# Kernel tuning notes

Measured on AMD Instinct MI355X. Metric: run time of the kernel, lower is better.

Reference implementation:

```python
import jax, jax.numpy as jnp
import numpy as np

DIM = 96       # d_model / channels
DSTATE = 16    # SSM state size N
DINNER = 2 * DIM   # expand=2 -> 192
DTRANK = 6     # ceil(DIM/16)
K = 4          # scan directions
B, H, W = 2, 56, 56


def _ln(x, g, b, eps=1e-5):
    m = x.mean(-1, keepdims=True)
    v = x.var(-1, keepdims=True)
    return (x - m) * jax.lax.rsqrt(v + eps) * g + b


def _dwconv3(x, w, b):  # x [B,C,H,W], w [C,1,3,3] depthwise, SAME padding
    y = jax.lax.conv_general_dilated(x, w, (1, 1), [(1, 1), (1, 1)],
                                     feature_group_count=x.shape[1],
                                     dimension_numbers=('NCHW', 'OIHW', 'NCHW'))
    return y + b[None, :, None, None]


def _bn(x, g, b, m, v, eps=1e-5):  # eval-mode BatchNorm2d on NCHW
    inv = jax.lax.rsqrt(v + eps)
    return (x - m[None, :, None, None]) * (inv * g)[None, :, None, None] + b[None, :, None, None]


def _selective_scan(u, dt, A, Bs, Cs, Dp, dt_bias):
    # u, dt: [B,K,D,L]; A: [K,D,N]; Bs,Cs: [B,K,N,L]; Dp, dt_bias: [K,D]
    dt = jax.nn.softplus(dt + dt_bias[None, :, :, None])
    dA = jnp.exp(jnp.einsum('bkdl,kdn->lbkdn', dt, A))           # [L,B,K,D,N]
    dBu = jnp.einsum('bkdl,bknl,bkdl->lbkdn', dt, Bs, u)          # [L,B,K,D,N]
    Ct = jnp.moveaxis(Cs, -1, 0)                                  # [L,B,K,N]
    h0 = jnp.zeros(dA.shape[1:], dA.dtype)

    def step(h, inp):
        dA_l, dBu_l, C_l = inp
        h = dA_l * h + dBu_l
        return h, jnp.einsum('bkdn,bkn->bkd', h, C_l)

    _, ys = jax.lax.scan(step, h0, (dA, dBu, Ct))                 # ys [L,B,K,D]
    return jnp.moveaxis(ys, 0, -1) + u * Dp[None, :, :, None]     # [B,K,D,L]


def setup_inputs() -> dict:
    key = jax.random.key(0)
    ks = jax.random.split(key, 12)
    s = 0.02
    f32 = jnp.float32
    inp = {}
    inp['x'] = jax.random.normal(ks[0], (B, H, W, DIM), f32)
    # conv branch: depthwise 3x3 + BN + ReLU + 1x1 + BN
    inp['dw_w'] = jax.random.normal(ks[1], (DIM, 1, 3, 3), f32) * s
    inp['dw_b'] = jnp.zeros((DIM,), f32)
    inp['bn1_g'] = jnp.ones((DIM,), f32); inp['bn1_b'] = jnp.zeros((DIM,), f32)
    inp['bn1_m'] = jnp.zeros((DIM,), f32); inp['bn1_v'] = jnp.ones((DIM,), f32)
    inp['pw_w'] = jax.random.normal(ks[2], (DIM, DIM), f32) * s
    inp['pw_b'] = jnp.zeros((DIM,), f32)
    inp['bn2_g'] = jnp.ones((DIM,), f32); inp['bn2_b'] = jnp.zeros((DIM,), f32)
    inp['bn2_m'] = jnp.zeros((DIM,), f32); inp['bn2_v'] = jnp.ones((DIM,), f32)
    # pre-mamba LayerNorm
    inp['ln_g'] = jnp.ones((DIM,), f32); inp['ln_b'] = jnp.zeros((DIM,), f32)
    # SS2D params
    inp['in_proj_w'] = jax.random.normal(ks[3], (2 * DINNER, DIM), f32) * s
    inp['conv_w'] = jax.random.normal(ks[4], (DINNER, 1, 3, 3), f32) * s
    inp['conv_b'] = jnp.zeros((DINNER,), f32)
    inp['x_proj_w'] = jax.random.normal(ks[5], (K, DTRANK + 2 * DSTATE, DINNER), f32) * s
    inp['dt_w'] = jax.random.normal(ks[6], (K, DINNER, DTRANK), f32) * s
    inp['dt_b'] = jnp.full((K, DINNER), -4.6, f32)  # softplus(dt_b) ~= 0.01
    inp['A_logs'] = jnp.log(jnp.tile(jnp.arange(1, DSTATE + 1, dtype=f32), (K * DINNER, 1)))
    inp['Ds'] = jnp.ones((K * DINNER,), f32)
    inp['out_norm_g'] = jnp.ones((DINNER,), f32); inp['out_norm_b'] = jnp.zeros((DINNER,), f32)
    inp['out_proj_w'] = jax.random.normal(ks[7], (DIM, DINNER), f32) * s
    # fusion: Linear(2*dim, dim) + LayerNorm(dim)
    inp['fus_w'] = jax.random.normal(ks[8], (DIM, 2 * DIM), f32) * s
    inp['fus_b'] = jnp.zeros((DIM,), f32)
    inp['fus_ln_g'] = jnp.ones((DIM,), f32); inp['fus_ln_b'] = jnp.zeros((DIM,), f32)
    return inp


def reference(x, dw_w, dw_b, bn1_g, bn1_b, bn1_m, bn1_v, pw_w, pw_b,
              bn2_g, bn2_b, bn2_m, bn2_v, ln_g, ln_b,
              in_proj_w, conv_w, conv_b, x_proj_w, dt_w, dt_b, A_logs, Ds,
              out_norm_g, out_norm_b, out_proj_w, fus_w, fus_b, fus_ln_g, fus_ln_b):
    Bsz, Hh, Ww, C = x.shape
    L = Hh * Ww
    # ----- conv branch -----
    xc = jnp.transpose(x, (0, 3, 1, 2))                       # [B,C,H,W]
    c = jax.nn.relu(_bn(_dwconv3(xc, dw_w, dw_b), bn1_g, bn1_b, bn1_m, bn1_v))
    c = jnp.einsum('bchw,oc->bohw', c, pw_w) + pw_b[None, :, None, None]
    conv_out = jnp.transpose(_bn(c, bn2_g, bn2_b, bn2_m, bn2_v), (0, 2, 3, 1))
    # ----- mamba (SS2D) branch -----
    xn = _ln(x, ln_g, ln_b)
    xz = xn @ in_proj_w.T                                     # [B,H,W,2*Din]
    xm, z = jnp.split(xz, 2, axis=-1)
    xm = jnp.transpose(xm, (0, 3, 1, 2))                      # [B,Din,H,W]
    xm = jax.nn.silu(_dwconv3(xm, conv_w, conv_b))
    v1 = xm.reshape(Bsz, DINNER, L)                           # row-major scan
    v2 = jnp.transpose(xm, (0, 1, 3, 2)).reshape(Bsz, DINNER, L)  # col-major scan
    xs = jnp.stack([v1, v2, v1[..., ::-1], v2[..., ::-1]], axis=1)  # [B,4,Din,L]
    x_dbl = jnp.einsum('bkdl,kcd->bkcl', xs, x_proj_w)
    dts, Bmat, Cmat = jnp.split(x_dbl, [DTRANK, DTRANK + DSTATE], axis=2)
    dts = jnp.einsum('bkrl,kdr->bkdl', dts, dt_w)
    A = -jnp.exp(A_logs).reshape(K, DINNER, DSTATE)
    out_y = _selective_scan(xs, dts, A, Bmat, Cmat, Ds.reshape(K, DINNER), dt_b)
    y1 = out_y[:, 0]
    inv_y = out_y[:, 2:4][..., ::-1]
    y2 = inv_y[:, 0]
    y3 = jnp.transpose(inv_y[:, 1].reshape(Bsz, DINNER, Ww, Hh), (0, 1, 3, 2)).reshape(Bsz, DINNER, L)
    y4 = jnp.transpose(out_y[:, 1].reshape(Bsz, DINNER, Ww, Hh), (0, 1, 3, 2)).reshape(Bsz, DINNER, L)
    y = jnp.transpose(y1 + y2 + y3 + y4, (0, 2, 1)).reshape(Bsz, Hh, Ww, DINNER)
    y = _ln(y, out_norm_g, out_norm_b)
    y = y * jax.nn.silu(z)
    mamba_out = y @ out_proj_w.T                              # [B,H,W,C]
    # ----- fusion + residual -----
    fused = jnp.concatenate([conv_out, mamba_out], axis=-1) @ fus_w.T + fus_b
    fused = _ln(fused, fus_ln_g, fus_ln_b)
    return x + fused
```

## Files before the change

kernel.cpp:

```cpp
#include <hip/hip_runtime.h>
#include <math.h>

#define BZ 2
#define HH 56
#define WW 56
#define LL 3136
#define CC 96
#define DI 192
#define NS 16
#define RR 6
#define NT 49
#define NC 49

#define OFF_CONV   0
#define OFF_XMRAW  602112
#define OFF_Z      1806336
#define OFF_V1     3010560
#define OFF_V2     4214784
#define OFF_DT     5419008
#define OFF_BS     10235904
#define OFF_CS     10637312
#define OFF_Y      11038720
#define OFF_Y13    15855616
#define OFF_T      18264064
#define OFF_W2     19468288

__device__ __forceinline__ float softplusf(float x) {
    if (x > 20.f) return x;
    return log1pf(__expf(x));
}

__global__ __launch_bounds__(64) void k0_w2(const float* __restrict__ fus_w,
                                            const float* __restrict__ opw,
                                            float* __restrict__ W2) {
    int i = blockIdx.x * 64 + threadIdx.x;
    if (i >= CC * DI) return;
    int o = i / DI, d = i % DI;
    float acc = 0.f;
    for (int j = 0; j < CC; ++j)
        acc += fus_w[o * DI + CC + j] * opw[j * DI + d];
    W2[i] = acc;
}

__global__ __launch_bounds__(256) void k0c_negA(const float* __restrict__ A_logs,
                                                float* __restrict__ negA) {
    int i = blockIdx.x * 256 + threadIdx.x;
    if (i < 4 * DI * NS) negA[i] = -__expf(A_logs[i]);
}

__global__ __launch_bounds__(256) void k1a_dw(const float* __restrict__ x,
    const float* __restrict__ dw_w, const float* __restrict__ dw_b,
    const float* __restrict__ bn1_g, const float* __restrict__ bn1_b,
    const float* __restrict__ bn1_m, const float* __restrict__ bn1_v,
    float* __restrict__ cbuf) {
    int i = blockIdx.x * 256 + threadIdx.x;
    if (i >= BZ * LL * CC) return;
    int c = i % CC;
    int bl = i / CC;
    int l = bl % LL, b = bl / LL;
    int h = l / WW, w = l % WW;
    float acc = dw_b[c];
    #pragma unroll
    for (int dy = -1; dy <= 1; ++dy) {
        int hh = h + dy; if (hh < 0 || hh >= HH) continue;
        #pragma unroll
        for (int dx = -1; dx <= 1; ++dx) {
            int ww = w + dx; if (ww < 0 || ww >= WW) continue;
            acc += x[((b * HH + hh) * WW + ww) * CC + c] * dw_w[c * 9 + (dy + 1) * 3 + (dx + 1)];
        }
    }
    float inv = rsqrtf(bn1_v[c] + 1e-5f);
    float v = (acc - bn1_m[c]) * inv * bn1_g[c] + bn1_b[c];
    cbuf[i] = fmaxf(v, 0.f);
}

__global__ __launch_bounds__(256) void k1b_pw(const float* __restrict__ cbuf,
    const float* __restrict__ pw_w, const float* __restrict__ pw_b,
    const float* __restrict__ bn2_g, const float* __restrict__ bn2_b,
    const float* __restrict__ bn2_m, const float* __restrict__ bn2_v,
    float* __restrict__ conv_out) {
    int t0 = blockIdx.x * 64;
    int b = blockIdx.y;
    int lane = threadIdx.x & 63;
    int wvu = __builtin_amdgcn_readfirstlane(threadIdx.x >> 6);
    __shared__ float ct[CC * 65];
    __shared__ float res[64 * 97];
    const float* cb = cbuf + (b * LL + t0) * CC;
    for (int e = threadIdx.x; e < 64 * CC; e += 256) {
        int p = e / CC, c = e % CC;
        ct[c * 65 + p] = cb[e];
    }
    __syncthreads();
    float acc[24];
    const float* pb = pw_b + wvu * 24;
    #pragma unroll
    for (int j = 0; j < 24; ++j) acc[j] = pb[j];
    const float* wb = pw_w + (wvu * 24) * CC;
    for (int c = 0; c < CC; ++c) {
        float xv = ct[c * 65 + lane];
        #pragma unroll
        for (int j = 0; j < 24; ++j)
            acc[j] += xv * wb[j * CC + c];
    }
    #pragma unroll
    for (int j = 0; j < 24; ++j) {
        int o = wvu * 24 + j;
        float inv = rsqrtf(bn2_v[o] + 1e-5f);
        res[lane * 97 + o] = (acc[j] - bn2_m[o]) * inv * bn2_g[o] + bn2_b[o];
    }
    __syncthreads();
    float* ob = conv_out + (b * LL + t0) * CC;
    for (int e = threadIdx.x; e < 64 * CC; e += 256) {
        int pl = e / CC, o = e % CC;
        ob[e] = res[pl * 97 + o];
    }
}

__global__ __launch_bounds__(256) void k2_inproj(const float* __restrict__ x,
    const float* __restrict__ ln_g, const float* __restrict__ ln_b,
    const float* __restrict__ ipw,
    float* __restrict__ xm_raw, float* __restrict__ z_buf) {
    int t0 = blockIdx.x * 64;
    int og = blockIdx.y;
    int b = blockIdx.z;
    int lane = threadIdx.x & 63;
    int wv = threadIdx.x >> 6;
    int wvu = __builtin_amdgcn_readfirstlane(wv);
    __shared__ float xt[64 * 97];
    __shared__ float xn[96 * 65];
    __shared__ float ps[4][64], ps2[4][64];
    const float* xb = x + (b * LL + t0) * CC;
    for (int e = threadIdx.x; e < 64 * CC; e += 256) {
        int p = e / CC, c = e % CC;
        xt[p * 97 + c] = xb[e];
    }
    __syncthreads();
    float s = 0.f, s2 = 0.f;
    #pragma unroll
    for (int j = 0; j < 24; ++j) {
        float v = xt[lane * 97 + wvu * 24 + j];
        s += v; s2 += v * v;
    }
    ps[wv][lane] = s; ps2[wv][lane] = s2;
    __syncthreads();
    float st = 0.f, st2 = 0.f;
    #pragma unroll
    for (int i = 0; i < 4; ++i) { st += ps[i][lane]; st2 += ps2[i][lane]; }
    float m = st * (1.f / 96.f);
    float inv = rsqrtf(st2 * (1.f / 96.f) - m * m + 1e-5f);
    #pragma unroll
    for (int j = 0; j < 24; ++j) {
        int c = wvu * 24 + j;
        xn[c * 65 + lane] = (xt[lane * 97 + c] - m) * inv * ln_g[c] + ln_b[c];
    }
    __syncthreads();
    float acc[24];
    #pragma unroll
    for (int j = 0; j < 24; ++j) acc[j] = 0.f;
    const float* wbase = ipw + (og * 96 + wvu * 24) * CC;
    for (int c = 0; c < CC; ++c) {
        float xv = xn[c * 65 + lane];
        #pragma unroll
        for (int j = 0; j < 24; ++j)
            acc[j] += xv * wbase[j * CC + c];
    }
    int p = t0 + lane;
    #pragma unroll
    for (int j = 0; j < 24; ++j) {
        int out = og * 96 + wvu * 24 + j;
        if (out < DI) xm_raw[(b * DI + out) * LL + p] = acc[j];
        else          z_buf[(b * DI + (out - DI)) * LL + p] = acc[j];
    }
}

__global__ __launch_bounds__(256) void k3_dw(const float* __restrict__ xm_raw,
    const float* __restrict__ conv_w, const float* __restrict__ conv_b,
    float* __restrict__ v1, float* __restrict__ v2) {
    int bd = blockIdx.x;
    int half = blockIdx.y;
    int d = bd % DI;
    int h0 = half * 28;
    __shared__ float tile[28 * 57];
    const float* src = xm_raw + bd * LL;
    float wloc[9];
    #pragma unroll
    for (int i = 0; i < 9; ++i) wloc[i] = conv_w[d * 9 + i];
    float bias = conv_b[d];
    for (int e = threadIdx.x; e < 28 * WW; e += 256) {
        int hl = e / WW, w = e % WW;
        int h = h0 + hl;
        float acc = bias;
        #pragma unroll
        for (int dy = -1; dy <= 1; ++dy) {
            int hh = h + dy; if (hh < 0 || hh >= HH) continue;
            #pragma unroll
            for (int dx = -1; dx <= 1; ++dx) {
                int ww = w + dx; if (ww < 0 || ww >= WW) continue;
                acc += src[hh * WW + ww] * wloc[(dy + 1) * 3 + (dx + 1)];
            }
        }
        float sig = 1.f / (1.f + __expf(-acc));
        float v = acc * sig;
        v1[bd * LL + h * WW + w] = v;
        tile[hl * 57 + w] = v;
    }
    __syncthreads();
    for (int e = threadIdx.x; e < 28 * WW; e += 256) {
        int w = e / 28, hl = e % 28;
        v2[bd * LL + w * HH + h0 + hl] = tile[hl * 57 + w];
    }
}

__global__ __launch_bounds__(256) void k4_proj(const float* __restrict__ v1,
    const float* __restrict__ v2, const float* __restrict__ xpw,
    const float* __restrict__ dtw, const float* __restrict__ dtb,
    float* __restrict__ dt_s, float* __restrict__ B_s, float* __restrict__ C_s) {
    int t0 = blockIdx.x * 64;
    int k = blockIdx.y;
    int b = blockIdx.z;
    int lane = threadIdx.x & 63;
    int wvu = __builtin_amdgcn_readfirstlane(threadIdx.x >> 6);
    __shared__ float xs_l[DI * 64];
    __shared__ float dtr[RR * 64];
    const float* src = ((k & 1) == 0 ? v1 : v2) + b * DI * LL + t0;
    for (int e = threadIdx.x; e < DI * 64; e += 256) {
        int d = e >> 6, p = e & 63;
        xs_l[e] = src[d * LL + p];
    }
    __syncthreads();
    int r0 = wvu * 10; if (r0 > 28) r0 = 28;
    float acc[10];
    #pragma unroll
    for (int i = 0; i < 10; ++i) acc[i] = 0.f;
    const float* wbase = xpw + (k * 38 + r0) * DI;
    for (int d = 0; d < DI; ++d) {
        float xv = xs_l[d * 64 + lane];
        #pragma unroll
        for (int i = 0; i < 10; ++i)
            acc[i] += xv * wbase[i * DI + d];
    }
    int p = t0 + lane;
    #pragma unroll
    for (int i = 0; i < 10; ++i) {
        int c = r0 + i;
        if (c < RR) {
            dtr[c * 64 + lane] = acc[i];
        } else if (c < RR + NS) {
            B_s[((b * 4 + k) * NS + (c - RR)) * LL + p] = acc[i];
        } else {
            C_s[((b * 4 + k) * NS + (c - RR - NS)) * LL + p] = acc[i];
        }
    }
    __syncthreads();
    for (int i = 0; i < 48; ++i) {
        int d = wvu * 48 + i;
        float a = dtb[k * DI + d];
        const float* wr = dtw + (k * DI + d) * RR;
        #pragma unroll
        for (int r = 0; r < RR; ++r)
            a += dtr[r * 64 + lane] * wr[r];
        dt_s[((b * 4 + k) * DI + d) * LL + p] = softplusf(a);
    }
}

__global__ __launch_bounds__(64) void k5a_scan(float* __restrict__ dt_s,
    const float* __restrict__ B_s, const float* __restrict__ C_s,
    const float* __restrict__ v1, const float* __restrict__ v2,
    const float* __restrict__ A_logs, float* __restrict__ y_scan,
    float* __restrict__ hlast) {
    int bx = blockIdx.x;
    int dg = bx % 3, c = bx / 3;
    int k = blockIdx.y, b = blockIdx.z;
    int bk = b * 4 + k;
    int lane = threadIdx.x;
    int d0 = dg * 64, d = d0 + lane;
    bool fwd = (k < 2);
    int s0 = fwd ? c * 64 : (LL - (c + 1) * 64);
    __shared__ float dt_l[64 * 65];
    __shared__ float u_l[64 * 65];
    __shared__ float4 bc4[64 * 9];
    float* bc = (float*)bc4;
    float Ae[16];
    const float* ap = A_logs + (k * DI + d) * NS;
    #pragma unroll
    for (int n = 0; n < 16; ++n) Ae[n] = -__expf(ap[n]) * 1.442695040888963f;
    const float* dtp = dt_s + (bk * DI + d0) * LL + s0;
    const float* up  = ((k == 0 || k == 2) ? v1 : v2) + (b * DI + d0) * LL + s0;
    #pragma unroll 8
    for (int r = 0; r < 64; ++r) {
        dt_l[r * 65 + lane] = dtp[r * LL + lane];
        u_l[r * 65 + lane]  = up[r * LL + lane];
    }
    const float* Bb = B_s + (bk * NS) * LL + s0;
    const float* Cb = C_s + (bk * NS) * LL + s0;
    #pragma unroll
    for (int n = 0; n < 16; ++n) {
        bc[lane * 36 + n]      = Bb[n * LL + lane];
        bc[lane * 36 + 16 + n] = Cb[n * LL + lane];
    }
    __syncthreads();
    float h[16];
    #pragma unroll
    for (int n = 0; n < 16; ++n) h[n] = 0.f;
    float cum = 0.f;
    for (int jj = 0; jj < 64; ++jj) {
        int j = fwd ? jj : 63 - jj;
        float dtv = dt_l[lane * 65 + j];
        float uv  = u_l[lane * 65 + j];
        float du = dtv * uv;
        cum += dtv;
        const float4* row = (const float4*)&bc[j * 36];
        float4 b0 = row[0], b1 = row[1], b2 = row[2], b3 = row[3];
        float4 c0 = row[4], c1 = row[5], c2 = row[6], c3 = row[7];
        float bv[16] = {b0.x,b0.y,b0.z,b0.w, b1.x,b1.y,b1.z,b1.w,
                        b2.x,b2.y,b2.z,b2.w, b3.x,b3.y,b3.z,b3.w};
        float cv[16] = {c0.x,c0.y,c0.z,c0.w, c1.x,c1.y,c1.z,c1.w,
                        c2.x,c2.y,c2.z,c2.w, c3.x,c3.y,c3.z,c3.w};
        float y = 0.f;
        #pragma unroll
        for (int n = 0; n < 16; ++n) {
            h[n] = exp2f(dtv * Ae[n]) * h[n] + du * bv[n];
            y += h[n] * cv[n];
        }
        u_l[lane * 65 + j] = y;
        dt_l[lane * 65 + j] = cum;
    }
    __syncthreads();
    float* yp = y_scan + (bk * DI + d0) * LL + s0;
    float* cp = dt_s + (bk * DI + d0) * LL + s0;
    #pragma unroll 8
    for (int r = 0; r < 64; ++r) {
        yp[r * LL + lane] = u_l[r * 65 + lane];
        cp[r * LL + lane] = dt_l[r * 65 + lane];
    }
    float4* hp4 = (float4*)(hlast + (bk * NC + c) * (DI * NS) + d * NS);
    hp4[0] = make_float4(h[0], h[1], h[2], h[3]);
    hp4[1] = make_float4(h[4], h[5], h[6], h[7]);
    hp4[2] = make_float4(h[8], h[9], h[10], h[11]);
    hp4[3] = make_float4(h[12], h[13], h[14], h[15]);
}

__global__ __launch_bounds__(64) void k5c_comb(const float* __restrict__ hlast,
    const float* __restrict__ cumdt, const float* __restrict__ negA,
    float* __restrict__ hin) {
    int dg = blockIdx.x, k = blockIdx.y, b = blockIdx.z;
    int lane = threadIdx.x, dl = lane >> 4, n = lane & 15;
    int d = dg * 4 + dl;
    int bk = b * 4 + k;
    bool fwd = (k < 2);
    float Av = negA[(k * DI + d) * NS + n];
    float H = 0.f;
    for (int c = 0; c < NC; ++c) {
        hin[(bk * NC + c) * (48 * 64) + dg * 64 + lane] = H;
        int s0 = fwd ? c * 64 : (LL - (c + 1) * 64);
        int jlast = fwd ? s0 + 63 : s0;
        float T = cumdt[(bk * DI + d) * LL + jlast];
        float hl = hlast[(bk * NC + c) * (48 * 64) + dg * 64 + lane];
        H = hl + __expf(Av * T) * H;
    }
}

__global__ __launch_bounds__(256) void k5d_corr(const float* __restrict__ cumdt,
    const float* __restrict__ C_s, const float* __restrict__ hin,
    const float* __restrict__ negA, float* __restrict__ y_scan) {
    int t = blockIdx.x;
    int k = blockIdx.y, b = blockIdx.z;
    bool fwd = (k < 2);
    int tile = fwd ? (t + 1) : t;
    int c = fwd ? tile : (48 - tile);
    int s0 = tile * 64;
    int lane = threadIdx.x & 63;
    int wvu = __builtin_amdgcn_readfirstlane(threadIdx.x >> 6);
    int bk = b * 4 + k;
    __shared__ float c_l[16 * 65];
    for (int e = threadIdx.x; e < 16 * 64; e += 256) {
        int n = e >> 6, s = e & 63;
        c_l[n * 65 + s] = C_s[(bk * NS + n) * LL + s0 + s];
    }
    __syncthreads();
    for (int dd = 0; dd < 48; ++dd) {
        int d = wvu * 48 + dd;
        float cd = cumdt[(bk * DI + d) * LL + s0 + lane];
        const float* hp = hin + (bk * NC + c) * (48 * 64) + d * 16;
        const float* ap = negA + (k * DI + d) * NS;
        float acc = 0.f;
        #pragma unroll
        for (int n = 0; n < 16; ++n) {
            acc += c_l[n * 65 + lane] * __expf(ap[n] * cd) * hp[n];
        }
        y_scan[(bk * DI + d) * LL + s0 + lane] += acc;
    }
}

__global__ __launch_bounds__(64) void k5b_tr(const float* __restrict__ y_scan,
                                             float* __restrict__ y13t) {
    int idx = blockIdx.x;
    int d = idx % DI;
    int bk = idx / DI;
    int kk = bk % 2, b = bk / 2;
    int k = (kk == 0) ? 1 : 3;
    __shared__ float tile[HH * 57];
    const float* src = y_scan + ((b * 4 + k) * DI + d) * LL;
    for (int e = threadIdx.x; e < LL; e += 64) {
        int w = e / HH, h = e % HH;
        tile[h * 57 + w] = src[e];
    }
    __syncthreads();
    float* dst = y13t + idx * LL;
    for (int e = threadIdx.x; e < LL; e += 64) {
        int h = e / WW, w = e % WW;
        dst[e] = tile[h * 57 + w];
    }
}

__global__ __launch_bounds__(256) void k6_gather(const float* __restrict__ y_scan,
    const float* __restrict__ y13t, const float* __restrict__ v1,
    const float* __restrict__ z_buf, const float* __restrict__ Ds,
    const float* __restrict__ ong, const float* __restrict__ onb,
    float* __restrict__ t_buf) {
    int t0 = blockIdx.x * 32;
    int b = blockIdx.y;
    int p32 = threadIdx.x & 31, sl = threadIdx.x >> 5;
    int p = t0 + p32;
    __shared__ float yv[DI * 33];
    __shared__ float ps[8][32], ps2[8][32];
    float s = 0.f, s2 = 0.f;
    for (int j = 0; j < 24; ++j) {
        int d = sl * 24 + j;
        float dsum = Ds[d] + Ds[DI + d] + Ds[2 * DI + d] + Ds[3 * DI + d];
        float val = y_scan[((b * 4 + 0) * DI + d) * LL + p]
                  + y_scan[((b * 4 + 2) * DI + d) * LL + p]
                  + y13t[((b * 2 + 0) * DI + d) * LL + p]
                  + y13t[((b * 2 + 1) * DI + d) * LL + p]
                  + v1[(b * DI + d) * LL + p] * dsum;
        yv[d * 33 + p32] = val;
        s += val; s2 += val * val;
    }
    ps[sl][p32] = s; ps2[sl][p32] = s2;
    __syncthreads();
    float st = 0.f, st2 = 0.f;
    #pragma unroll
    for (int i = 0; i < 8; ++i) { st += ps[i][p32]; st2 += ps2[i][p32]; }
    float m = st * (1.f / 192.f);
    float inv = rsqrtf(st2 * (1.f / 192.f) - m * m + 1e-5f);
    for (int j = 0; j < 24; ++j) {
        int d = sl * 24 + j;
        float val = (yv[d * 33 + p32] - m) * inv * ong[d] + onb[d];
        float zz = z_buf[(b * DI + d) * LL + p];
        float sig = 1.f / (1.f + __expf(-zz));
        t_buf[(b * DI + d) * LL + p] = val * zz * sig;
    }
}

__global__ __launch_bounds__(256) void k7a_mm(const float* __restrict__ t_buf,
    const float* __restrict__ conv_out, const float* __restrict__ W2,
    const float* __restrict__ fus_w, const float* __restrict__ fus_b,
    float* __restrict__ fusedT) {
    int t0 = blockIdx.x * 64;
    int og = blockIdx.y;
    int b = blockIdx.z;
    int lane = threadIdx.x & 63;
    int wvu = __builtin_amdgcn_readfirstlane(threadIdx.x >> 6);
    __shared__ float ct[CC * 65];
    const float* cb = conv_out + (b * LL + t0) * CC;
    for (int e = threadIdx.x; e < 64 * CC; e += 256) {
        int p = e / CC, c = e % CC;
        ct[c * 65 + p] = cb[e];
    }
    __syncthreads();
    int o0 = og * 24 + wvu * 6;
    float acc[6];
    #pragma unroll
    for (int j = 0; j < 6; ++j) acc[j] = fus_b[o0 + j];
    int p = t0 + lane;
    const float* w2 = W2 + o0 * DI;
    for (int d = 0; d < DI; ++d) {
        float tv = t_buf[(b * DI + d) * LL + p];
        #pragma unroll
        for (int j = 0; j < 6; ++j)
            acc[j] += tv * w2[j * DI + d];
    }
    const float* fw = fus_w + o0 * DI;
    for (int c = 0; c < CC; ++c) {
        float cv = ct[c * 65 + lane];
        #pragma unroll
        for (int j = 0; j < 6; ++j)
            acc[j] += cv * fw[j * DI + c];
    }
    #pragma unroll
    for (int j = 0; j < 6; ++j)
        fusedT[(b * CC + o0 + j) * LL + p] = acc[j];
}

__global__ __launch_bounds__(256) void k7b_ln(const float* __restrict__ fusedT,
    const float* __restrict__ flg, const float* __restrict__ flb,
    const float* __restrict__ x, float* __restrict__ out) {
    int t0 = blockIdx.x * 64;
    int b = blockIdx.y;
    int lane = threadIdx.x & 63, wv = threadIdx.x >> 6;
    __shared__ float ft[CC * 65];
    __shared__ float res[64 * 97];
    __shared__ float ps[4][64], ps2[4][64];
    for (int e = threadIdx.x; e < CC * 64; e += 256) {
        int o = e >> 6, p = e & 63;
        ft[o * 65 + p] = fusedT[(b * CC + o) * LL + t0 + p];
    }
    __syncthreads();
    float s = 0.f, s2 = 0.f;
    #pragma unroll
    for (int j = 0; j < 24; ++j) {
        float v = ft[(wv * 24 + j) * 65 + lane];
        s += v; s2 += v * v;
    }
    ps[wv][lane] = s; ps2[wv][lane] = s2;
    __syncthreads();
    float st = 0.f, st2 = 0.f;
    #pragma unroll
    for (int i = 0; i < 4; ++i) { st += ps[i][lane]; st2 += ps2[i][lane]; }
    float m = st * (1.f / 96.f);
    float inv = rsqrtf(st2 * (1.f / 96.f) - m * m + 1e-5f);
    #pragma unroll
    for (int j = 0; j < 24; ++j) {
        int o = wv * 24 + j;
        res[lane * 97 + o] = (ft[o * 65 + lane] - m) * inv * flg[o] + flb[o];
    }
    __syncthreads();
    const float* xb = x + (b * LL + t0) * CC;
    float* ob = out + (b * LL + t0) * CC;
    for (int e = threadIdx.x; e < 64 * CC; e += 256) {
        int pl = e / CC, o = e % CC;
        ob[e] = xb[e] + res[pl * 97 + o];
    }
}

extern "C" void kernel_launch(void* const* d_in, const int* in_sizes, int n_in,
                              void* d_out, int out_size, void* d_ws, size_t ws_size,
                              hipStream_t stream) {
    const float* x        = (const float*)d_in[0];
    const float* dw_w     = (const float*)d_in[1];
    const float* dw_b     = (const float*)d_in[2];
    const float* bn1_g    = (const float*)d_in[3];
    const float* bn1_b    = (const float*)d_in[4];
    const float* bn1_m    = (const float*)d_in[5];
    const float* bn1_v    = (const float*)d_in[6];
    const float* pw_w     = (const float*)d_in[7];
    const float* pw_b     = (const float*)d_in[8];
    const float* bn2_g    = (const float*)d_in[9];
    const float* bn2_b    = (const float*)d_in[10];
    const float* bn2_m    = (const float*)d_in[11];
    const float* bn2_v    = (const float*)d_in[12];
    const float* ln_g     = (const float*)d_in[13];
    const float* ln_b     = (const float*)d_in[14];
    const float* ipw      = (const float*)d_in[15];
    const float* conv_w   = (const float*)d_in[16];
    const float* conv_b   = (const float*)d_in[17];
    const float* xpw      = (const float*)d_in[18];
    const float* dtw      = (const float*)d_in[19];
    const float* dtb      = (const float*)d_in[20];
    const float* A_logs   = (const float*)d_in[21];
    const float* Ds       = (const float*)d_in[22];
    const float* ong      = (const float*)d_in[23];
    const float* onb      = (const float*)d_in[24];
    const float* opw      = (const float*)d_in[25];
    const float* fus_w    = (const float*)d_in[26];
    const float* fus_b    = (const float*)d_in[27];
    const float* flg      = (const float*)d_in[28];
    const float* flb      = (const float*)d_in[29];

    float* ws = (float*)d_ws;
    float* conv_out = ws + OFF_CONV;
    float* xm_raw   = ws + OFF_XMRAW;
    float* z_buf    = ws + OFF_Z;
    float* v1       = ws + OFF_V1;
    float* v2       = ws + OFF_V2;
    float* dt_s     = ws + OFF_DT;
    float* B_s      = ws + OFF_BS;
    float* C_s      = ws + OFF_CS;
    float* y_scan   = ws + OFF_Y;
    float* y13t     = ws + OFF_Y13;
    float* t_buf    = ws + OFF_T;
    float* W2       = ws + OFF_W2;
    float* hlast    = xm_raw;
    float* hin      = t_buf;
    float* negA     = B_s;
    float* cbuf     = y13t;
    float* fusedT   = y13t;
    float* out      = (float*)d_out;

    k0_w2<<<dim3((CC * DI + 63) / 64), dim3(64), 0, stream>>>(fus_w, opw, W2);
    k1a_dw<<<dim3((BZ * LL * CC + 255) / 256), dim3(256), 0, stream>>>(x, dw_w, dw_b,
                                                     bn1_g, bn1_b, bn1_m, bn1_v, cbuf);
    k1b_pw<<<dim3(NT, BZ), dim3(256), 0, stream>>>(cbuf, pw_w, pw_b,
                                                   bn2_g, bn2_b, bn2_m, bn2_v, conv_out);
    k2_inproj<<<dim3(NT, 4, BZ), dim3(256), 0, stream>>>(x, ln_g, ln_b, ipw, xm_raw, z_buf);
    k3_dw<<<dim3(BZ * DI, 2), dim3(256), 0, stream>>>(xm_raw, conv_w, conv_b, v1, v2);
    k4_proj<<<dim3(NT, 4, BZ), dim3(256), 0, stream>>>(v1, v2, xpw, dtw, dtb, dt_s, B_s, C_s);
    k5a_scan<<<dim3(3 * NC, 4, BZ), dim3(64), 0, stream>>>(dt_s, B_s, C_s, v1, v2, A_logs, y_scan, hlast);
    k0c_negA<<<dim3(48), dim3(256), 0, stream>>>(A_logs, negA);
    k5c_comb<<<dim3(48, 4, BZ), dim3(64), 0, stream>>>(hlast, dt_s, negA, hin);
    k5d_corr<<<dim3(48, 4, BZ), dim3(256), 0, stream>>>(dt_s, C_s, hin, negA, y_scan);
    k5b_tr<<<dim3(BZ * 2 * DI), dim3(64), 0, stream>>>(y_scan, y13t);
    k6_gather<<<dim3(2 * NT, BZ), dim3(256), 0, stream>>>(y_scan, y13t, v1, z_buf, Ds, ong, onb, t_buf);
    k7a_mm<<<dim3(NT, 4, BZ), dim3(256), 0, stream>>>(t_buf, conv_out, W2, fus_w, fus_b, fusedT);
    k7b_ln<<<dim3(NT, BZ), dim3(256), 0, stream>>>(fusedT, flg, flb, x, out);
}
```

Measured before the change: 381.0 us.

## Halve scan chunk length and recompute cumulative dt in correction pass

The chunked selective scan now uses 32-step chunks instead of 64, doubling the number of scan blocks and shortening each block's serial dependency chain. Chunk carry-out states are written into a larger reused buffer along with a single per-chunk dt total, so the scan no longer writes a full cumulative-dt array. The correction kernel rebuilds the in-chunk cumulative dt with a wave-level shuffle prefix sum. The combine kernel's serial pass doubles in length, and the transpose kernel moves to 256 threads.

```diff
diff --git a/kernel.cpp b/kernel.cpp
--- a/kernel.cpp
+++ b/kernel.cpp
@@ -10,7 +10,8 @@
 #define NS 16
 #define RR 6
 #define NT 49
-#define NC 49
+#define NCH 98
+#define CH 32
 
 #define OFF_CONV   0
 #define OFF_XMRAW  602112
@@ -263,11 +264,11 @@
     }
 }
 
-__global__ __launch_bounds__(64) void k5a_scan(float* __restrict__ dt_s,
+__global__ __launch_bounds__(64) void k5a_scan(const float* __restrict__ dt_s,
     const float* __restrict__ B_s, const float* __restrict__ C_s,
     const float* __restrict__ v1, const float* __restrict__ v2,
     const float* __restrict__ A_logs, float* __restrict__ y_scan,
-    float* __restrict__ hlast) {
+    float* __restrict__ hl_buf, float* __restrict__ Tbuf) {
     int bx = blockIdx.x;
     int dg = bx % 3, c = bx / 3;
     int k = blockIdx.y, b = blockIdx.z;
@@ -275,43 +276,43 @@
     int lane = threadIdx.x;
     int d0 = dg * 64, d = d0 + lane;
     bool fwd = (k < 2);
-    int s0 = fwd ? c * 64 : (LL - (c + 1) * 64);
-    __shared__ float dt_l[64 * 65];
-    __shared__ float u_l[64 * 65];
-    __shared__ float4 bc4[64 * 9];
-    float* bc = (float*)bc4;
+    int s0 = fwd ? c * CH : (LL - (c + 1) * CH);
+    __shared__ float dtl[64 * 33];
+    __shared__ float ul[64 * 33];
+    __shared__ float bc[CH * 36];
     float Ae[16];
     const float* ap = A_logs + (k * DI + d) * NS;
     #pragma unroll
     for (int n = 0; n < 16; ++n) Ae[n] = -__expf(ap[n]) * 1.442695040888963f;
     const float* dtp = dt_s + (bk * DI + d0) * LL + s0;
-    const float* up  = ((k == 0 || k == 2) ? v1 : v2) + (b * DI + d0) * LL + s0;
+    const float* up  = ((k & 1) == 0 ? v1 : v2) + (b * DI + d0) * LL + s0;
+    int pr = lane >> 5, pc = lane & 31;
     #pragma unroll 8
-    for (int r = 0; r < 64; ++r) {
-        dt_l[r * 65 + lane] = dtp[r * LL + lane];
-        u_l[r * 65 + lane]  = up[r * LL + lane];
-    }
-    const float* Bb = B_s + (bk * NS) * LL + s0;
-    const float* Cb = C_s + (bk * NS) * LL + s0;
-    #pragma unroll
-    for (int n = 0; n < 16; ++n) {
-        bc[lane * 36 + n]      = Bb[n * LL + lane];
-        bc[lane * 36 + 16 + n] = Cb[n * LL + lane];
+    for (int i = 0; i < 32; ++i) {
+        int row = i * 2 + pr;
+        dtl[row * 33 + pc] = dtp[row * LL + pc];
+        ul[row * 33 + pc]  = up[row * LL + pc];
+    }
+    #pragma unroll
+    for (int i = 0; i < 8; ++i) {
+        int nn = i * 2 + pr;
+        bc[pc * 36 + nn]      = B_s[(bk * NS + nn) * LL + s0 + pc];
+        bc[pc * 36 + 16 + nn] = C_s[(bk * NS + nn) * LL + s0 + pc];
     }
     __syncthreads();
     float h[16];
     #pragma unroll
     for (int n = 0; n < 16; ++n) h[n] = 0.f;
     float cum = 0.f;
-    for (int jj = 0; jj < 64; ++jj) {
-        int j = fwd ? jj : 63 - jj;
-        float dtv = dt_l[lane * 65 + j];
-        float uv  = u_l[lane * 65 + j];
+    for (int jj = 0; jj < CH; ++jj) {
+        int j = fwd ? jj : CH - 1 - jj;
+        float dtv = dtl[lane * 33 + j];
+        float uv  = ul[lane * 33 + j];
         float du = dtv * uv;
         cum += dtv;
-        const float4* row = (const float4*)&bc[j * 36];
-        float4 b0 = row[0], b1 = row[1], b2 = row[2], b3 = row[3];
-        float4 c0 = row[4], c1 = row[5], c2 = row[6], c3 = row[7];
+        const float4* row4 = (const float4*)&bc[j * 36];
+        float4 b0 = row4[0], b1 = row4[1], b2 = row4[2], b3 = row4[3];
+        float4 c0 = row4[4], c1 = row4[5], c2 = row4[6], c3 = row4[7];
         float bv[16] = {b0.x,b0.y,b0.z,b0.w, b1.x,b1.y,b1.z,b1.w,
                         b2.x,b2.y,b2.z,b2.w, b3.x,b3.y,b3.z,b3.w};
         float cv[16] = {c0.x,c0.y,c0.z,c0.w, c1.x,c1.y,c1.z,c1.w,
@@ -322,78 +323,86 @@
             h[n] = exp2f(dtv * Ae[n]) * h[n] + du * bv[n];
             y += h[n] * cv[n];
         }
-        u_l[lane * 65 + j] = y;
-        dt_l[lane * 65 + j] = cum;
+        ul[lane * 33 + j] = y;
     }
     __syncthreads();
     float* yp = y_scan + (bk * DI + d0) * LL + s0;
-    float* cp = dt_s + (bk * DI + d0) * LL + s0;
     #pragma unroll 8
-    for (int r = 0; r < 64; ++r) {
-        yp[r * LL + lane] = u_l[r * 65 + lane];
-        cp[r * LL + lane] = dt_l[r * 65 + lane];
-    }
-    float4* hp4 = (float4*)(hlast + (bk * NC + c) * (DI * NS) + d * NS);
+    for (int i = 0; i < 32; ++i) {
+        int row = i * 2 + pr;
+        yp[row * LL + pc] = ul[row * 33 + pc];
+    }
+    float4* hp4 = (float4*)(hl_buf + (bk * NCH + c) * (DI * NS) + d * NS);
     hp4[0] = make_float4(h[0], h[1], h[2], h[3]);
     hp4[1] = make_float4(h[4], h[5], h[6], h[7]);
     hp4[2] = make_float4(h[8], h[9], h[10], h[11]);
     hp4[3] = make_float4(h[12], h[13], h[14], h[15]);
-}
-
-__global__ __launch_bounds__(64) void k5c_comb(const float* __restrict__ hlast,
-    const float* __restrict__ cumdt, const float* __restrict__ negA,
-    float* __restrict__ hin) {
+    Tbuf[(bk * NCH + c) * DI + d] = cum;
+}
+
+__global__ __launch_bounds__(64) void k5c_comb(float* __restrict__ hl_buf,
+    const float* __restrict__ Tbuf, const float* __restrict__ negA) {
     int dg = blockIdx.x, k = blockIdx.y, b = blockIdx.z;
     int lane = threadIdx.x, dl = lane >> 4, n = lane & 15;
     int d = dg * 4 + dl;
     int bk = b * 4 + k;
-    bool fwd = (k < 2);
     float Av = negA[(k * DI + d) * NS + n];
     float H = 0.f;
-    for (int c = 0; c < NC; ++c) {
-        hin[(bk * NC + c) * (48 * 64) + dg * 64 + lane] = H;
-        int s0 = fwd ? c * 64 : (LL - (c + 1) * 64);
-        int jlast = fwd ? s0 + 63 : s0;
-        float T = cumdt[(bk * DI + d) * LL + jlast];
-        float hl = hlast[(bk * NC + c) * (48 * 64) + dg * 64 + lane];
+    for (int c = 0; c < NCH; ++c) {
+        float* slot = hl_buf + (bk * NCH + c) * (DI * NS) + dg * 64 + lane;
+        float hl = *slot;
+        *slot = H;
+        float T = Tbuf[(bk * NCH + c) * DI + d];
         H = hl + __expf(Av * T) * H;
     }
 }
 
-__global__ __launch_bounds__(256) void k5d_corr(const float* __restrict__ cumdt,
+__global__ __launch_bounds__(256) void k5d_corr(const float* __restrict__ dt_s,
     const float* __restrict__ C_s, const float* __restrict__ hin,
     const float* __restrict__ negA, float* __restrict__ y_scan) {
     int t = blockIdx.x;
     int k = blockIdx.y, b = blockIdx.z;
     bool fwd = (k < 2);
-    int tile = fwd ? (t + 1) : t;
-    int c = fwd ? tile : (48 - tile);
-    int s0 = tile * 64;
-    int lane = threadIdx.x & 63;
-    int wvu = __builtin_amdgcn_readfirstlane(threadIdx.x >> 6);
+    int c  = fwd ? (t + 1) : (NCH - 1 - t);
+    int s0 = fwd ? (t + 1) * CH : t * CH;
+    int p32 = threadIdx.x & 31, sl = threadIdx.x >> 5;
     int bk = b * 4 + k;
-    __shared__ float c_l[16 * 65];
-    for (int e = threadIdx.x; e < 16 * 64; e += 256) {
-        int n = e >> 6, s = e & 63;
-        c_l[n * 65 + s] = C_s[(bk * NS + n) * LL + s0 + s];
-    }
-    __syncthreads();
-    for (int dd = 0; dd < 48; ++dd) {
-        int d = wvu * 48 + dd;
-        float cd = cumdt[(bk * DI + d) * LL + s0 + lane];
-        const float* hp = hin + (bk * NC + c) * (48 * 64) + d * 16;
+    __shared__ float c_l[16 * 33];
+    for (int e = threadIdx.x; e < 16 * CH; e += 256) {
+        int n = e >> 5, s = e & 31;
+        c_l[n * 33 + s] = C_s[(bk * NS + n) * LL + s0 + s];
+    }
+    __syncthreads();
+    for (int j = 0; j < 24; ++j) {
+        int d = sl * 24 + j;
+        float dtv = dt_s[(bk * DI + d) * LL + s0 + p32];
+        float cum = dtv;
+        if (fwd) {
+            #pragma unroll
+            for (int off = 1; off < 32; off <<= 1) {
+                float o = __shfl_up(cum, off, 32);
+                if (p32 >= off) cum += o;
+            }
+        } else {
+            #pragma unroll
+            for (int off = 1; off < 32; off <<= 1) {
+                float o = __shfl_down(cum, off, 32);
+                if (p32 < 32 - off) cum += o;
+            }
+        }
+        const float* hp = hin + (bk * NCH + c) * (DI * NS) + d * 16;
         const float* ap = negA + (k * DI + d) * NS;
         float acc = 0.f;
         #pragma unroll
         for (int n = 0; n < 16; ++n) {
-            acc += c_l[n * 65 + lane] * __expf(ap[n] * cd) * hp[n];
+            acc += c_l[n * 33 + p32] * __expf(ap[n] * cum) * hp[n];
         }
-        y_scan[(bk * DI + d) * LL + s0 + lane] += acc;
-    }
-}
-
-__global__ __launch_bounds__(64) void k5b_tr(const float* __restrict__ y_scan,
-                                             float* __restrict__ y13t) {
+        y_scan[(bk * DI + d) * LL + s0 + p32] += acc;
+    }
+}
+
+__global__ __launch_bounds__(256) void k5b_tr(const float* __restrict__ y_scan,
+                                              float* __restrict__ y13t) {
     int idx = blockIdx.x;
     int d = idx % DI;
     int bk = idx / DI;
@@ -401,13 +410,13 @@
     int k = (kk == 0) ? 1 : 3;
     __shared__ float tile[HH * 57];
     const float* src = y_scan + ((b * 4 + k) * DI + d) * LL;
-    for (int e = threadIdx.x; e < LL; e += 64) {
+    for (int e = threadIdx.x; e < LL; e += 256) {
         int w = e / HH, h = e % HH;
         tile[h * 57 + w] = src[e];
     }
     __syncthreads();
     float* dst = y13t + idx * LL;
-    for (int e = threadIdx.x; e < LL; e += 64) {
+    for (int e = threadIdx.x; e < LL; e += 256) {
         int h = e / WW, w = e % WW;
         dst[e] = tile[h * 57 + w];
     }
@@ -580,10 +589,10 @@
     float* y13t     = ws + OFF_Y13;
     float* t_buf    = ws + OFF_T;
     float* W2       = ws + OFF_W2;
-    float* hlast    = xm_raw;
-    float* hin      = t_buf;
+    float* cbuf     = y13t;
+    float* hl_buf   = y13t;
+    float* Tbuf     = xm_raw;
     float* negA     = B_s;
-    float* cbuf     = y13t;
     float* fusedT   = y13t;
     float* out      = (float*)d_out;
 
@@ -595,11 +604,12 @@
     k2_inproj<<<dim3(NT, 4, BZ), dim3(256), 0, stream>>>(x, ln_g, ln_b, ipw, xm_raw, z_buf);
     k3_dw<<<dim3(BZ * DI, 2), dim3(256), 0, stream>>>(xm_raw, conv_w, conv_b, v1, v2);
     k4_proj<<<dim3(NT, 4, BZ), dim3(256), 0, stream>>>(v1, v2, xpw, dtw, dtb, dt_s, B_s, C_s);
-    k5a_scan<<<dim3(3 * NC, 4, BZ), dim3(64), 0, stream>>>(dt_s, B_s, C_s, v1, v2, A_logs, y_scan, hlast);
+    k5a_scan<<<dim3(3 * NCH, 4, BZ), dim3(64), 0, stream>>>(dt_s, B_s, C_s, v1, v2, A_logs,
+                                                            y_scan, hl_buf, Tbuf);
     k0c_negA<<<dim3(48), dim3(256), 0, stream>>>(A_logs, negA);
-    k5c_comb<<<dim3(48, 4, BZ), dim3(64), 0, stream>>>(hlast, dt_s, negA, hin);
-    k5d_corr<<<dim3(48, 4, BZ), dim3(256), 0, stream>>>(dt_s, C_s, hin, negA, y_scan);
-    k5b_tr<<<dim3(BZ * 2 * DI), dim3(64), 0, stream>>>(y_scan, y13t);
+    k5c_comb<<<dim3(48, 4, BZ), dim3(64), 0, stream>>>(hl_buf, Tbuf, negA);
+    k5d_corr<<<dim3(NCH - 1, 4, BZ), dim3(256), 0, stream>>>(dt_s, C_s, hl_buf, negA, y_scan);
+    k5b_tr<<<dim3(BZ * 2 * DI), dim3(256), 0, stream>>>(y_scan, y13t);
     k6_gather<<<dim3(2 * NT, BZ), dim3(256), 0, stream>>>(y_scan, y13t, v1, z_buf, Ds, ong, onb, t_buf);
     k7a_mm<<<dim3(NT, 4, BZ), dim3(256), 0, stream>>>(t_buf, conv_out, W2, fus_w, fus_b, fusedT);
     k7b_ln<<<dim3(NT, BZ), dim3(256), 0, stream>>>(fusedT, flg, flb, x, out);
```

Result: faster. 372.0 us (-2.4%).
